# Kernel optimization log

Hardware: AMD Instinct MI355X
Metric: run time of the kernel (lower is better)

The kernel has to match this reference:

```python
import jax, jax.numpy as jnp
import numpy as np

B, S, D = 4, 2048, 1024

def _xavier(key, shape):
    bound = float(np.sqrt(6.0 / (shape[0] + shape[1])))
    return jax.random.uniform(key, shape, dtype=jnp.float32, minval=-bound, maxval=bound)

def setup_inputs() -> dict:
    key = jax.random.key(0)
    k0, k1, k2, k3 = jax.random.split(key, 4)
    return {
        "embeddings": jax.random.normal(k0, (B, S, D), dtype=jnp.float32),
        "W_Q": _xavier(k1, (D, D)),
        "W_K": _xavier(k2, (D, D)),
        "W_V": _xavier(k3, (D, D)),
    }

def reference(embeddings, W_Q, W_K, W_V):
    _, seq_len, d = embeddings.shape
    Q = embeddings @ W_Q                      # [B,S,D]
    K = embeddings @ W_K
    V = embeddings @ W_V
    scale = 1.0 / jnp.sqrt(jnp.float32(d))
    scores = jnp.einsum('bqd,bkd->bqk', Q, K) * scale   # [B,S,S]
    causal = jnp.tril(jnp.ones((seq_len, seq_len), dtype=bool))
    scores = jnp.where(causal[None, :, :], scores, -jnp.inf)
    probs = jax.nn.softmax(scores, axis=-1)
    return jnp.einsum('bqk,bkd->bqd', probs, V)
```

## Files before the change

### kernel.cpp

```cpp
#include <hip/hip_runtime.h>
#include <hip/hip_bf16.h>

#define BSZ 4
#define SEQ 2048
#define DIM 1024

typedef __attribute__((ext_vector_type(8))) short bf16x8;
typedef __attribute__((ext_vector_type(4))) float floatx4;

__device__ __forceinline__ unsigned short f2bf(float x) {
  union { float f; unsigned int u; } v; v.f = x;
  unsigned int r = v.u + 0x7fffu + ((v.u >> 16) & 1u);
  return (unsigned short)(r >> 16);
}

template <typename T> __device__ __forceinline__ void store_c(T* p, float v);
template <> __device__ __forceinline__ void store_c<float>(float* p, float v) { *p = v; }
template <> __device__ __forceinline__ void store_c<unsigned short>(unsigned short* p, float v) { *p = f2bf(v); }

__global__ __launch_bounds__(256) void cast_e(const float* __restrict__ in,
                                              unsigned short* __restrict__ out, int n) {
  int i = (blockIdx.x * 256 + threadIdx.x) * 4;
  if (i >= n) return;
  float4 v = *(const float4*)(in + i);
  ushort4 o;
  o.x = f2bf(v.x); o.y = f2bf(v.y); o.z = f2bf(v.z); o.w = f2bf(v.w);
  *(ushort4*)(out + i) = o;
}

__global__ __launch_bounds__(256) void transpose_w(const float* __restrict__ Wq,
                                                   const float* __restrict__ Wk,
                                                   const float* __restrict__ Wv,
                                                   unsigned short* __restrict__ WtQK,
                                                   unsigned short* __restrict__ WtV) {
  __shared__ float tile[32][33];
  int z = blockIdx.z;
  const float* W = (z == 0) ? Wq : (z == 1) ? Wk : Wv;
  unsigned short* dst = (z == 2) ? WtV : WtQK;
  int row_off = (z == 1) ? 1024 : 0;
  int n0 = blockIdx.x * 32, k0 = blockIdx.y * 32;
  int tx = threadIdx.x, ty = threadIdx.y;
  for (int r = ty; r < 32; r += 8)
    tile[r][tx] = W[(size_t)(k0 + r) * DIM + n0 + tx];
  __syncthreads();
  for (int r = ty; r < 32; r += 8)
    dst[(size_t)(row_off + n0 + r) * DIM + k0 + tx] = f2bf(tile[tx][r]);
}

__global__ __launch_bounds__(256) void proj_dual(
    const unsigned short* __restrict__ Ebf,
    const unsigned short* __restrict__ WtQK,
    const unsigned short* __restrict__ WtV,
    unsigned short* __restrict__ QKo,
    unsigned short* __restrict__ Vt) {
  const unsigned short *A, *B;
  unsigned short* C;
  int lda, ldb, ldc, m0, n0;
  int x = blockIdx.x;
  if (x < 1024) {
    m0 = (x >> 4) * 128; n0 = (x & 15) * 128;
    A = Ebf; lda = DIM; B = WtQK; ldb = DIM; C = QKo; ldc = 2 * DIM;
  } else {
    x -= 1024;
    m0 = (x >> 6) * 128; n0 = (x & 63) * 128;
    A = WtV; lda = DIM; B = Ebf; ldb = DIM; C = Vt; ldc = BSZ * SEQ;
  }
  const int Keff = DIM;

  __shared__ __align__(16) unsigned short As[128][72];
  __shared__ __align__(16) unsigned short Bs[128][72];

  int tid = threadIdx.x;
  int lane = tid & 63;
  int wid = tid >> 6;
  int wm = (wid >> 1) * 64, wn = (wid & 1) * 64;
  int lr = lane & 15, lq = lane >> 4;
  int row = tid >> 3;
  int kc = (tid & 7) * 8;

  const unsigned short* Ab = A + (size_t)(m0 + row) * lda + kc;
  const unsigned short* Bb = B + (size_t)(n0 + row) * ldb + kc;
  size_t la = (size_t)32 * lda, lb = (size_t)32 * ldb;

  uint4 ra0 = *(const uint4*)(Ab);
  uint4 ra1 = *(const uint4*)(Ab + la);
  uint4 ra2 = *(const uint4*)(Ab + 2 * la);
  uint4 ra3 = *(const uint4*)(Ab + 3 * la);
  uint4 rb0 = *(const uint4*)(Bb);
  uint4 rb1 = *(const uint4*)(Bb + lb);
  uint4 rb2 = *(const uint4*)(Bb + 2 * lb);
  uint4 rb3 = *(const uint4*)(Bb + 3 * lb);

  floatx4 acc[4][4] = {};

  for (int k0 = 0; k0 < Keff; k0 += 64) {
    __syncthreads();
    *(uint4*)&As[row][kc]      = ra0;
    *(uint4*)&As[row + 32][kc] = ra1;
    *(uint4*)&As[row + 64][kc] = ra2;
    *(uint4*)&As[row + 96][kc] = ra3;
    *(uint4*)&Bs[row][kc]      = rb0;
    *(uint4*)&Bs[row + 32][kc] = rb1;
    *(uint4*)&Bs[row + 64][kc] = rb2;
    *(uint4*)&Bs[row + 96][kc] = rb3;
    if (k0 + 64 < Keff) {
      const unsigned short* An = Ab + k0 + 64;
      const unsigned short* Bn = Bb + k0 + 64;
      ra0 = *(const uint4*)(An);
      ra1 = *(const uint4*)(An + la);
      ra2 = *(const uint4*)(An + 2 * la);
      ra3 = *(const uint4*)(An + 3 * la);
      rb0 = *(const uint4*)(Bn);
      rb1 = *(const uint4*)(Bn + lb);
      rb2 = *(const uint4*)(Bn + 2 * lb);
      rb3 = *(const uint4*)(Bn + 3 * lb);
    }
    __syncthreads();
#pragma unroll
    for (int kk = 0; kk < 64; kk += 32) {
      bf16x8 af[4], bfr[4];
      int kl = kk + lq * 8;
#pragma unroll
      for (int i = 0; i < 4; i++) af[i] = *(const bf16x8*)&As[wm + i * 16 + lr][kl];
#pragma unroll
      for (int j = 0; j < 4; j++) bfr[j] = *(const bf16x8*)&Bs[wn + j * 16 + lr][kl];
#pragma unroll
      for (int i = 0; i < 4; i++)
#pragma unroll
        for (int j = 0; j < 4; j++)
          acc[i][j] = __builtin_amdgcn_mfma_f32_16x16x32_bf16(af[i], bfr[j], acc[i][j], 0, 0, 0);
    }
  }

#pragma unroll
  for (int i = 0; i < 4; i++) {
    int rbase = m0 + wm + i * 16 + lq * 4;
#pragma unroll
    for (int j = 0; j < 4; j++) {
      int col = n0 + wn + j * 16 + lr;
#pragma unroll
      for (int r = 0; r < 4; r++)
        C[(size_t)(rbase + r) * ldc + col] = f2bf(acc[i][j][r]);
    }
  }
}

template <typename OutT, int MODE>
__global__ __launch_bounds__(256) void gemm_nt(
    const unsigned short* __restrict__ A, int lda, long long strideA,
    const unsigned short* __restrict__ B, int ldb, long long strideB,
    OutT* __restrict__ C, int ldc, long long strideC,
    int Kdim, float scale, float* __restrict__ rowsum) {
  int m0, n0;
  if constexpr (MODE == 1) {
    int t = blockIdx.x;
    int mt = 0;
    while (((mt + 1) * (mt + 2)) / 2 <= t) mt++;
    int nt = t - (mt * (mt + 1)) / 2;
    m0 = mt * 128; n0 = nt * 128;
  } else {
    m0 = (gridDim.y - 1 - blockIdx.y) * 128;
    n0 = blockIdx.x * 128;
  }
  int Keff = (MODE == 2) ? min(Kdim, m0 + 128) : Kdim;
  A += (long long)blockIdx.z * strideA;
  B += (long long)blockIdx.z * strideB;
  C += (long long)blockIdx.z * strideC;
  rowsum += (size_t)blockIdx.z * SEQ;

  __shared__ __align__(16) unsigned short As[128][72];
  __shared__ __align__(16) unsigned short Bs[128][72];

  int tid = threadIdx.x;
  int lane = tid & 63;
  int wid = tid >> 6;
  int wm = (wid >> 1) * 64, wn = (wid & 1) * 64;
  int lr = lane & 15, lq = lane >> 4;
  int row = tid >> 3;
  int kc = (tid & 7) * 8;

  const unsigned short* Ab = A + (size_t)(m0 + row) * lda + kc;
  const unsigned short* Bb = B + (size_t)(n0 + row) * ldb + kc;
  size_t la = (size_t)32 * lda, lb = (size_t)32 * ldb;

  uint4 ra0 = *(const uint4*)(Ab);
  uint4 ra1 = *(const uint4*)(Ab + la);
  uint4 ra2 = *(const uint4*)(Ab + 2 * la);
  uint4 ra3 = *(const uint4*)(Ab + 3 * la);
  uint4 rb0 = *(const uint4*)(Bb);
  uint4 rb1 = *(const uint4*)(Bb + lb);
  uint4 rb2 = *(const uint4*)(Bb + 2 * lb);
  uint4 rb3 = *(const uint4*)(Bb + 3 * lb);

  floatx4 acc[4][4] = {};

  for (int k0 = 0; k0 < Keff; k0 += 64) {
    __syncthreads();
    *(uint4*)&As[row][kc]      = ra0;
    *(uint4*)&As[row + 32][kc] = ra1;
    *(uint4*)&As[row + 64][kc] = ra2;
    *(uint4*)&As[row + 96][kc] = ra3;
    *(uint4*)&Bs[row][kc]      = rb0;
    *(uint4*)&Bs[row + 32][kc] = rb1;
    *(uint4*)&Bs[row + 64][kc] = rb2;
    *(uint4*)&Bs[row + 96][kc] = rb3;
    if (k0 + 64 < Keff) {
      const unsigned short* An = Ab + k0 + 64;
      const unsigned short* Bn = Bb + k0 + 64;
      ra0 = *(const uint4*)(An);
      ra1 = *(const uint4*)(An + la);
      ra2 = *(const uint4*)(An + 2 * la);
      ra3 = *(const uint4*)(An + 3 * la);
      rb0 = *(const uint4*)(Bn);
      rb1 = *(const uint4*)(Bn + lb);
      rb2 = *(const uint4*)(Bn + 2 * lb);
      rb3 = *(const uint4*)(Bn + 3 * lb);
    }
    __syncthreads();
#pragma unroll
    for (int kk = 0; kk < 64; kk += 32) {
      bf16x8 af[4], bfr[4];
      int kl = kk + lq * 8;
#pragma unroll
      for (int i = 0; i < 4; i++) af[i] = *(const bf16x8*)&As[wm + i * 16 + lr][kl];
#pragma unroll
      for (int j = 0; j < 4; j++) bfr[j] = *(const bf16x8*)&Bs[wn + j * 16 + lr][kl];
#pragma unroll
      for (int i = 0; i < 4; i++)
#pragma unroll
        for (int j = 0; j < 4; j++)
          acc[i][j] = __builtin_amdgcn_mfma_f32_16x16x32_bf16(af[i], bfr[j], acc[i][j], 0, 0, 0);
    }
  }

  if constexpr (MODE == 1) {
#pragma unroll
    for (int i = 0; i < 4; i++) {
      int rbase = m0 + wm + i * 16 + lq * 4;
      float s0 = 0.f, s1 = 0.f, s2 = 0.f, s3 = 0.f;
#pragma unroll
      for (int j = 0; j < 4; j++) {
        int col = n0 + wn + j * 16 + lr;
        float e0 = (col <= rbase + 0) ? __expf(acc[i][j][0] * scale) : 0.0f;
        float e1 = (col <= rbase + 1) ? __expf(acc[i][j][1] * scale) : 0.0f;
        float e2 = (col <= rbase + 2) ? __expf(acc[i][j][2] * scale) : 0.0f;
        float e3 = (col <= rbase + 3) ? __expf(acc[i][j][3] * scale) : 0.0f;
        store_c(&C[(size_t)(rbase + 0) * ldc + col], e0);
        store_c(&C[(size_t)(rbase + 1) * ldc + col], e1);
        store_c(&C[(size_t)(rbase + 2) * ldc + col], e2);
        store_c(&C[(size_t)(rbase + 3) * ldc + col], e3);
        s0 += e0; s1 += e1; s2 += e2; s3 += e3;
      }
#pragma unroll
      for (int m = 1; m < 16; m <<= 1) {
        s0 += __shfl_xor(s0, m, 64);
        s1 += __shfl_xor(s1, m, 64);
        s2 += __shfl_xor(s2, m, 64);
        s3 += __shfl_xor(s3, m, 64);
      }
      if (lr == 0) {
        atomicAdd(&rowsum[rbase + 0], s0);
        atomicAdd(&rowsum[rbase + 1], s1);
        atomicAdd(&rowsum[rbase + 2], s2);
        atomicAdd(&rowsum[rbase + 3], s3);
      }
    }
  } else {
#pragma unroll
    for (int i = 0; i < 4; i++) {
      int rbase = m0 + wm + i * 16 + lq * 4;
      float i0 = 1.0f / rowsum[rbase + 0];
      float i1 = 1.0f / rowsum[rbase + 1];
      float i2 = 1.0f / rowsum[rbase + 2];
      float i3 = 1.0f / rowsum[rbase + 3];
#pragma unroll
      for (int j = 0; j < 4; j++) {
        int col = n0 + wn + j * 16 + lr;
        store_c(&C[(size_t)(rbase + 0) * ldc + col], acc[i][j][0] * i0);
        store_c(&C[(size_t)(rbase + 1) * ldc + col], acc[i][j][1] * i1);
        store_c(&C[(size_t)(rbase + 2) * ldc + col], acc[i][j][2] * i2);
        store_c(&C[(size_t)(rbase + 3) * ldc + col], acc[i][j][3] * i3);
      }
    }
  }
}

extern "C" void kernel_launch(void* const* d_in, const int* in_sizes, int n_in,
                              void* d_out, int out_size, void* d_ws, size_t ws_size,
                              hipStream_t stream) {
  const float* E  = (const float*)d_in[0];
  const float* Wq = (const float*)d_in[1];
  const float* Wk = (const float*)d_in[2];
  const float* Wv = (const float*)d_in[3];
  float* out = (float*)d_out;

  char* ws = (char*)d_ws;
  size_t off = 0;
  auto alloc = [&](size_t bytes) {
    void* p = ws + off;
    off += (bytes + 255) & ~(size_t)255;
    return p;
  };
  const size_t M_ALL = (size_t)BSZ * SEQ;
  unsigned short* Ebf  = (unsigned short*)alloc(M_ALL * DIM * 2);
  unsigned short* WtQK = (unsigned short*)alloc((size_t)2 * DIM * DIM * 2);
  unsigned short* WtV  = (unsigned short*)alloc((size_t)DIM * DIM * 2);
  unsigned short* QK   = (unsigned short*)alloc(M_ALL * 2 * DIM * 2);
  unsigned short* Vt   = (unsigned short*)alloc((size_t)DIM * M_ALL * 2);
  unsigned short* ExpS = (unsigned short*)alloc((size_t)BSZ * SEQ * SEQ * 2);
  float*          Rsum = (float*)alloc((size_t)BSZ * SEQ * 4);

  int nE = (int)(M_ALL * DIM);
  cast_e<<<dim3(nE / (256 * 4)), dim3(256), 0, stream>>>(E, Ebf, nE);
  transpose_w<<<dim3(32, 32, 3), dim3(32, 8), 0, stream>>>(Wq, Wk, Wv, WtQK, WtV);
  hipMemsetAsync(Rsum, 0, (size_t)BSZ * SEQ * 4, stream);

  proj_dual<<<dim3(1536), dim3(256), 0, stream>>>(Ebf, WtQK, WtV, QK, Vt);

  gemm_nt<unsigned short, 1><<<dim3(136, 1, BSZ), dim3(256), 0, stream>>>(
      QK, 2 * DIM, (long long)SEQ * 2 * DIM,
      QK + DIM, 2 * DIM, (long long)SEQ * 2 * DIM,
      ExpS, SEQ, (long long)SEQ * SEQ,
      DIM, 0.03125f , Rsum);

  gemm_nt<float, 2><<<dim3(8, 16, BSZ), dim3(256), 0, stream>>>(
      ExpS, SEQ, (long long)SEQ * SEQ,
      Vt, (int)M_ALL, (long long)SEQ,
      out, DIM, (long long)SEQ * DIM,
      SEQ, 1.0f, Rsum);
}
```

Before: 244.4 us.

## Rewrite projection GEMM with 256x256 tiles and async LDS multi-stage pipeline

The projection kernel is replaced by one that computes 256x256 output tiles with 512 threads, loads global data straight into shared memory through global_load_lds, and keeps a four-deep ring of K-slices in flight with explicit vmcnt waits and barriers. MFMA phases are interleaved with the next stage's loads and run under raised wave priority. This targets the projection GEMM's global-load latency and the register round-trip staging of the old 128x128 kernel. The cost is much higher register use for the 8x4 accumulator array, a fragile hand-written wait schedule, and fewer blocks (384) across the device.

```diff
diff --git a/kernel.cpp b/kernel.cpp
--- a/kernel.cpp
+++ b/kernel.cpp
@@ -47,7 +47,15 @@
     dst[(size_t)(row_off + n0 + r) * DIM + k0 + tx] = f2bf(tile[tx][r]);
 }
 
-__global__ __launch_bounds__(256) void proj_dual(
+__device__ __forceinline__ void gload16(const unsigned short* g, unsigned short* l) {
+  __builtin_amdgcn_global_load_lds(
+      (const __attribute__((address_space(1))) unsigned int*)g,
+      (__attribute__((address_space(3))) unsigned int*)l, 16, 0, 0);
+}
+
+#define NT_PROJ 32
+
+__global__ __launch_bounds__(512, 2) void proj256(
     const unsigned short* __restrict__ Ebf,
     const unsigned short* __restrict__ WtQK,
     const unsigned short* __restrict__ WtV,
@@ -55,17 +63,122 @@
     unsigned short* __restrict__ Vt) {
   const unsigned short *A, *B;
   unsigned short* C;
-  int lda, ldb, ldc, m0, n0;
+  int ldc, m0, n0;
   int x = blockIdx.x;
-  if (x < 1024) {
-    m0 = (x >> 4) * 128; n0 = (x & 15) * 128;
-    A = Ebf; lda = DIM; B = WtQK; ldb = DIM; C = QKo; ldc = 2 * DIM;
+  if (x < 256) {
+    m0 = (x >> 3) * 256; n0 = (x & 7) * 256;
+    A = Ebf; B = WtQK; C = QKo; ldc = 2 * DIM;
   } else {
-    x -= 1024;
-    m0 = (x >> 6) * 128; n0 = (x & 63) * 128;
-    A = WtV; lda = DIM; B = Ebf; ldb = DIM; C = Vt; ldc = BSZ * SEQ;
-  }
-  const int Keff = DIM;
+    x -= 256;
+    m0 = (x >> 5) * 256; n0 = (x & 31) * 256;
+    A = WtV; B = Ebf; C = Vt; ldc = BSZ * SEQ;
+  }
+
+  __shared__ __align__(16) unsigned short sA[4][256][32];
+  __shared__ __align__(16) unsigned short sB[4][256][32];
+
+  const int tid = threadIdx.x;
+  const int lane = tid & 63;
+  const int wid = tid >> 6;
+  const int wm = (wid >> 2) * 128;
+  const int wn = (wid & 3) * 64;
+  const int lr = lane & 15, lq = lane >> 4;
+
+  const unsigned short* gA = A + (size_t)(m0 + (tid >> 2)) * DIM + (tid & 3) * 8;
+  const unsigned short* gB = B + (size_t)(n0 + (tid >> 2)) * DIM + (tid & 3) * 8;
+  unsigned short* lA = &sA[0][16 * wid][0];
+  unsigned short* lB = &sB[0][16 * wid][0];
+  const size_t swG = (size_t)128 * DIM;
+
+#define STAGE_A(T) do { int rb_ = (T) & 3; \
+    gload16(gA + (size_t)(T) * 32,       lA + rb_ * 8192); \
+    gload16(gA + (size_t)(T) * 32 + swG, lA + rb_ * 8192 + 4096); } while (0)
+#define STAGE_B(T) do { int rb_ = (T) & 3; \
+    gload16(gB + (size_t)(T) * 32,       lB + rb_ * 8192); \
+    gload16(gB + (size_t)(T) * 32 + swG, lB + rb_ * 8192 + 4096); } while (0)
+
+  floatx4 acc[8][4] = {};
+
+  STAGE_A(0); STAGE_B(0);
+  STAGE_A(1); STAGE_B(1);
+  STAGE_A(2); STAGE_B(2);
+  asm volatile("s_waitcnt vmcnt(8)" ::: "memory");
+  __builtin_amdgcn_s_barrier();
+
+#pragma unroll 1
+  for (int T = 0; T < NT_PROJ; ++T) {
+    asm volatile("" ::: "memory");
+    const int rb = T & 3;
+    bf16x8 af[4], bfr[4];
+#pragma unroll
+    for (int j = 0; j < 4; ++j) bfr[j] = *(const bf16x8*)&sB[rb][wn + j * 16 + lr][lq * 8];
+#pragma unroll
+    for (int i = 0; i < 4; ++i) af[i] = *(const bf16x8*)&sA[rb][wm + i * 16 + lr][lq * 8];
+    if (T + 3 < NT_PROJ) STAGE_A(T + 3);
+    __builtin_amdgcn_s_barrier();
+    __builtin_amdgcn_s_setprio(1);
+#pragma unroll
+    for (int i = 0; i < 4; ++i)
+#pragma unroll
+      for (int j = 0; j < 4; ++j)
+        acc[i][j] = __builtin_amdgcn_mfma_f32_16x16x32_bf16(af[i], bfr[j], acc[i][j], 0, 0, 0);
+    __builtin_amdgcn_s_setprio(0);
+    __builtin_amdgcn_s_barrier();
+#pragma unroll
+    for (int i = 0; i < 4; ++i) af[i] = *(const bf16x8*)&sA[rb][wm + 64 + i * 16 + lr][lq * 8];
+    if (T + 3 < NT_PROJ) STAGE_B(T + 3);
+    __builtin_amdgcn_s_barrier();
+    __builtin_amdgcn_s_setprio(1);
+#pragma unroll
+    for (int i = 0; i < 4; ++i)
+#pragma unroll
+      for (int j = 0; j < 4; ++j)
+        acc[4 + i][j] = __builtin_amdgcn_mfma_f32_16x16x32_bf16(af[i], bfr[j], acc[4 + i][j], 0, 0, 0);
+    __builtin_amdgcn_s_setprio(0);
+    if (T < NT_PROJ - 3)       { asm volatile("s_waitcnt vmcnt(8)" ::: "memory"); }
+    else if (T == NT_PROJ - 3) { asm volatile("s_waitcnt vmcnt(4)" ::: "memory"); }
+    else if (T == NT_PROJ - 2) { asm volatile("s_waitcnt vmcnt(0)" ::: "memory"); }
+    else                       { asm volatile("" ::: "memory"); }
+    __builtin_amdgcn_s_barrier();
+  }
+#undef STAGE_A
+#undef STAGE_B
+
+#pragma unroll
+  for (int i = 0; i < 8; ++i) {
+    int rbase = m0 + wm + i * 16 + lq * 4;
+#pragma unroll
+    for (int j = 0; j < 4; ++j) {
+      int col = n0 + wn + j * 16 + lr;
+#pragma unroll
+      for (int r = 0; r < 4; ++r)
+        C[(size_t)(rbase + r) * ldc + col] = f2bf(acc[i][j][r]);
+    }
+  }
+}
+
+template <typename OutT, int MODE>
+__global__ __launch_bounds__(256) void gemm_nt(
+    const unsigned short* __restrict__ A, int lda, long long strideA,
+    const unsigned short* __restrict__ B, int ldb, long long strideB,
+    OutT* __restrict__ C, int ldc, long long strideC,
+    int Kdim, float scale, float* __restrict__ rowsum) {
+  int m0, n0;
+  if constexpr (MODE == 1) {
+    int t = blockIdx.x;
+    int mt = 0;
+    while (((mt + 1) * (mt + 2)) / 2 <= t) mt++;
+    int nt = t - (mt * (mt + 1)) / 2;
+    m0 = mt * 128; n0 = nt * 128;
+  } else {
+    m0 = (gridDim.y - 1 - blockIdx.y) * 128;
+    n0 = blockIdx.x * 128;
+  }
+  int Keff = (MODE == 2) ? min(Kdim, m0 + 128) : Kdim;
+  A += (long long)blockIdx.z * strideA;
+  B += (long long)blockIdx.z * strideB;
+  C += (long long)blockIdx.z * strideC;
+  rowsum += (size_t)blockIdx.z * SEQ;
 
   __shared__ __align__(16) unsigned short As[128][72];
   __shared__ __align__(16) unsigned short Bs[128][72];
@@ -132,107 +245,6 @@
     }
   }
 
-#pragma unroll
-  for (int i = 0; i < 4; i++) {
-    int rbase = m0 + wm + i * 16 + lq * 4;
-#pragma unroll
-    for (int j = 0; j < 4; j++) {
-      int col = n0 + wn + j * 16 + lr;
-#pragma unroll
-      for (int r = 0; r < 4; r++)
-        C[(size_t)(rbase + r) * ldc + col] = f2bf(acc[i][j][r]);
-    }
-  }
-}
-
-template <typename OutT, int MODE>
-__global__ __launch_bounds__(256) void gemm_nt(
-    const unsigned short* __restrict__ A, int lda, long long strideA,
-    const unsigned short* __restrict__ B, int ldb, long long strideB,
-    OutT* __restrict__ C, int ldc, long long strideC,
-    int Kdim, float scale, float* __restrict__ rowsum) {
-  int m0, n0;
-  if constexpr (MODE == 1) {
-    int t = blockIdx.x;
-    int mt = 0;
-    while (((mt + 1) * (mt + 2)) / 2 <= t) mt++;
-    int nt = t - (mt * (mt + 1)) / 2;
-    m0 = mt * 128; n0 = nt * 128;
-  } else {
-    m0 = (gridDim.y - 1 - blockIdx.y) * 128;
-    n0 = blockIdx.x * 128;
-  }
-  int Keff = (MODE == 2) ? min(Kdim, m0 + 128) : Kdim;
-  A += (long long)blockIdx.z * strideA;
-  B += (long long)blockIdx.z * strideB;
-  C += (long long)blockIdx.z * strideC;
-  rowsum += (size_t)blockIdx.z * SEQ;
-
-  __shared__ __align__(16) unsigned short As[128][72];
-  __shared__ __align__(16) unsigned short Bs[128][72];
-
-  int tid = threadIdx.x;
-  int lane = tid & 63;
-  int wid = tid >> 6;
-  int wm = (wid >> 1) * 64, wn = (wid & 1) * 64;
-  int lr = lane & 15, lq = lane >> 4;
-  int row = tid >> 3;
-  int kc = (tid & 7) * 8;
-
-  const unsigned short* Ab = A + (size_t)(m0 + row) * lda + kc;
-  const unsigned short* Bb = B + (size_t)(n0 + row) * ldb + kc;
-  size_t la = (size_t)32 * lda, lb = (size_t)32 * ldb;
-
-  uint4 ra0 = *(const uint4*)(Ab);
-  uint4 ra1 = *(const uint4*)(Ab + la);
-  uint4 ra2 = *(const uint4*)(Ab + 2 * la);
-  uint4 ra3 = *(const uint4*)(Ab + 3 * la);
-  uint4 rb0 = *(const uint4*)(Bb);
-  uint4 rb1 = *(const uint4*)(Bb + lb);
-  uint4 rb2 = *(const uint4*)(Bb + 2 * lb);
-  uint4 rb3 = *(const uint4*)(Bb + 3 * lb);
-
-  floatx4 acc[4][4] = {};
-
-  for (int k0 = 0; k0 < Keff; k0 += 64) {
-    __syncthreads();
-    *(uint4*)&As[row][kc]      = ra0;
-    *(uint4*)&As[row + 32][kc] = ra1;
-    *(uint4*)&As[row + 64][kc] = ra2;
-    *(uint4*)&As[row + 96][kc] = ra3;
-    *(uint4*)&Bs[row][kc]      = rb0;
-    *(uint4*)&Bs[row + 32][kc] = rb1;
-    *(uint4*)&Bs[row + 64][kc] = rb2;
-    *(uint4*)&Bs[row + 96][kc] = rb3;
-    if (k0 + 64 < Keff) {
-      const unsigned short* An = Ab + k0 + 64;
-      const unsigned short* Bn = Bb + k0 + 64;
-      ra0 = *(const uint4*)(An);
-      ra1 = *(const uint4*)(An + la);
-      ra2 = *(const uint4*)(An + 2 * la);
-      ra3 = *(const uint4*)(An + 3 * la);
-      rb0 = *(const uint4*)(Bn);
-      rb1 = *(const uint4*)(Bn + lb);
-      rb2 = *(const uint4*)(Bn + 2 * lb);
-      rb3 = *(const uint4*)(Bn + 3 * lb);
-    }
-    __syncthreads();
-#pragma unroll
-    for (int kk = 0; kk < 64; kk += 32) {
-      bf16x8 af[4], bfr[4];
-      int kl = kk + lq * 8;
-#pragma unroll
-      for (int i = 0; i < 4; i++) af[i] = *(const bf16x8*)&As[wm + i * 16 + lr][kl];
-#pragma unroll
-      for (int j = 0; j < 4; j++) bfr[j] = *(const bf16x8*)&Bs[wn + j * 16 + lr][kl];
-#pragma unroll
-      for (int i = 0; i < 4; i++)
-#pragma unroll
-        for (int j = 0; j < 4; j++)
-          acc[i][j] = __builtin_amdgcn_mfma_f32_16x16x32_bf16(af[i], bfr[j], acc[i][j], 0, 0, 0);
-    }
-  }
-
   if constexpr (MODE == 1) {
 #pragma unroll
     for (int i = 0; i < 4; i++) {
@@ -315,7 +327,7 @@
   transpose_w<<<dim3(32, 32, 3), dim3(32, 8), 0, stream>>>(Wq, Wk, Wv, WtQK, WtV);
   hipMemsetAsync(Rsum, 0, (size_t)BSZ * SEQ * 4, stream);
 
-  proj_dual<<<dim3(1536), dim3(256), 0, stream>>>(Ebf, WtQK, WtV, QK, Vt);
+  proj256<<<dim3(384), dim3(512), 0, stream>>>(Ebf, WtQK, WtV, QK, Vt);
 
   gemm_nt<unsigned short, 1><<<dim3(136, 1, BSZ), dim3(256), 0, stream>>>(
       QK, 2 * DIM, (long long)SEQ * 2 * DIM,
```

New measurement: 258.8 us. 1.06x slower.
